# Optimization experiments

Hardware: AMD Instinct MI355X
Metric: run time of the kernel (lower is better)

The kernel has to match this reference:

```python
import jax, jax.numpy as jnp
import numpy as np

B, N, C = 8, 16384, 512

def setup_inputs() -> dict:
    key = jax.random.key(0)
    k1, k2 = jax.random.split(key)
    x = jax.random.normal(k1, (B, N, C), dtype=jnp.float32)
    gamma = jax.random.normal(k2, (1,), dtype=jnp.float32)
    return {"x": x, "gamma": gamma}

def reference(x, gamma):
    # x: [B, N, C]; torch code permutes to [B, C, N] for q/k/v
    v = jnp.transpose(x, (0, 2, 1))            # [B, C, N]
    # energy[b, i, j] = sum_n v[b, i, n] * v[b, j, n]  -> [B, C, C]
    energy = jnp.einsum('bin,bjn->bij', v, v)
    # max-subtract-then-negate score transform
    energy_new = jnp.max(energy, axis=-1, keepdims=True) - energy
    attention = jax.nn.softmax(energy_new, axis=-1)   # [B, C, C]
    out = jnp.einsum('bij,bjn->bin', attention, v)    # [B, C, N]
    out = gamma * out + v
    return jnp.transpose(out, (0, 2, 1))              # [B, N, C]
```

## Files before the change

### kernel.cpp

```cpp
#include <hip/hip_runtime.h>
#include <hip/hip_fp16.h>
#include <stdint.h>

#define B_ 8
#define N_ 16384
#define C_ 512
#define KS 16

typedef _Float16 h16;
typedef _Float16 half8 __attribute__((ext_vector_type(8)));
typedef float f32x4 __attribute__((ext_vector_type(4)));

__device__ __forceinline__ void gload16(const void* g, void* l) {
  __builtin_amdgcn_global_load_lds(
      (const __attribute__((address_space(1))) uint32_t*)g,
      (__attribute__((address_space(3))) uint32_t*)l, 16, 0, 0);
}

__device__ __forceinline__ half8 ldfrag(const h16* t, int r, int g) {
  return *(const half8*)(t + r * 32 + ((g ^ ((r >> 1) & 3)) << 3));
}

__global__ __launch_bounds__(256) void k_prep(const float* __restrict__ x,
    h16* __restrict__ xtH, h16* __restrict__ xtL, h16* __restrict__ xh, int b0) {
  int bl = blockIdx.z, b = b0 + bl;
  int n0 = blockIdx.x << 6, c0 = blockIdx.y << 6;
  __shared__ __align__(16) h16 lh[64][70];
  __shared__ __align__(16) h16 ll[64][70];
  int t = threadIdx.x;
  const float* xp = x + ((size_t)b * N_ + n0) * C_ + c0;
  h16* xhp = xh + ((size_t)bl * N_ + n0) * C_ + c0;
#pragma unroll
  for (int it = 0; it < 4; ++it) {
    int nr = (t >> 4) + (it << 4);
    int c4 = (t & 15) << 2;
    f32x4 v = *(const f32x4*)(xp + (size_t)nr * C_ + c4);
    h16 hv[4], lv[4];
#pragma unroll
    for (int u = 0; u < 4; ++u) {
      h16 h = (h16)v[u];
      hv[u] = h;
      lv[u] = (h16)(v[u] - (float)h);
    }
    union { h16 a[4]; uint2 u2; } ph;
    ph.a[0] = hv[0]; ph.a[1] = hv[1]; ph.a[2] = hv[2]; ph.a[3] = hv[3];
    *(uint2*)(xhp + (size_t)nr * C_ + c4) = ph.u2;
#pragma unroll
    for (int u = 0; u < 4; ++u) { lh[c4 + u][nr] = hv[u]; ll[c4 + u][nr] = lv[u]; }
  }
  __syncthreads();
  int cr = t >> 2, ns = (t & 3) << 4;
  size_t ob = ((size_t)bl * C_ + c0 + cr) * N_ + n0 + ns;
  uint32_t rh[8], rl[8];
#pragma unroll
  for (int e = 0; e < 8; ++e) {
    rh[e] = *(const uint32_t*)&lh[cr][ns + 2 * e];
    rl[e] = *(const uint32_t*)&ll[cr][ns + 2 * e];
  }
  *(uint4*)(xtH + ob)     = make_uint4(rh[0], rh[1], rh[2], rh[3]);
  *(uint4*)(xtH + ob + 8) = make_uint4(rh[4], rh[5], rh[6], rh[7]);
  *(uint4*)(xtL + ob)     = make_uint4(rl[0], rl[1], rl[2], rl[3]);
  *(uint4*)(xtL + ob + 8) = make_uint4(rl[4], rl[5], rl[6], rl[7]);
}

__global__ __launch_bounds__(256) void k_gram(const h16* __restrict__ xtH,
    const h16* __restrict__ xtL, float* __restrict__ Ep, int nb) {
  int NW = gridDim.x;
  int b = blockIdx.x;
  int L = (b & 7) * (NW >> 3) + (b >> 3);
  int tp = L % 10;
  int pair = L / 10;
  int kq = pair & (KS - 1);
  int bl = pair / KS;
  int ti = 0, rem = tp;
  while (rem >= 4 - ti) { rem -= 4 - ti; ++ti; }
  int tj = ti + rem;
  int i0 = ti << 7, j0 = tj << 7;
  bool diag = (ti == tj);
  int k0 = kq * (N_ / KS);
  __shared__ __align__(16) h16 lds[4 * 4096];
  const h16* bHi = xtH + ((size_t)bl * C_ + i0) * N_;
  const h16* bLi = xtL + ((size_t)bl * C_ + i0) * N_;
  const h16* bHj = xtH + ((size_t)bl * C_ + j0) * N_;
  const h16* bLj = xtL + ((size_t)bl * C_ + j0) * N_;
  int tid = threadIdx.x, lane = tid & 63, wid = tid >> 6;
  int wr = (wid >> 1) << 6, wc = (wid & 1) << 6;
  int r16 = lane & 15, g = lane >> 4;
  f32x4 acc[4][4] = {};
  const h16* pHi = lds;
  const h16* pLi = lds + 4096;
  const h16* pHj = diag ? lds : lds + 8192;
  const h16* pLj = diag ? lds + 4096 : lds + 12288;
  int r0 = tid >> 2, s = tid & 3;
  int r1 = r0 + 64;
  int sx0 = (s ^ ((r0 >> 1) & 3)) << 3, sx1 = (s ^ ((r1 >> 1) & 3)) << 3;
  int d0 = r0 * 32 + s * 8, d1 = r1 * 32 + s * 8;
  for (int kc = 0; kc < N_ / KS / 32; ++kc) {
    int k = k0 + (kc << 5);
    __syncthreads();
    gload16(bHi + (size_t)r0 * N_ + k + sx0, (void*)(lds + d0));
    gload16(bHi + (size_t)r1 * N_ + k + sx1, (void*)(lds + d1));
    gload16(bLi + (size_t)r0 * N_ + k + sx0, (void*)(lds + 4096 + d0));
    gload16(bLi + (size_t)r1 * N_ + k + sx1, (void*)(lds + 4096 + d1));
    if (!diag) {
      gload16(bHj + (size_t)r0 * N_ + k + sx0, (void*)(lds + 8192 + d0));
      gload16(bHj + (size_t)r1 * N_ + k + sx1, (void*)(lds + 8192 + d1));
      gload16(bLj + (size_t)r0 * N_ + k + sx0, (void*)(lds + 12288 + d0));
      gload16(bLj + (size_t)r1 * N_ + k + sx1, (void*)(lds + 12288 + d1));
    }
    __syncthreads();
    half8 ahi[4], ali[4], bhj[4], blj[4];
#pragma unroll
    for (int m = 0; m < 4; ++m) {
      int ra = wr + (m << 4) + r16;
      int rb = wc + (m << 4) + r16;
      ahi[m] = ldfrag(pHi, ra, g);
      ali[m] = ldfrag(pLi, ra, g);
      bhj[m] = ldfrag(pHj, rb, g);
      blj[m] = ldfrag(pLj, rb, g);
    }
#pragma unroll
    for (int m = 0; m < 4; ++m)
#pragma unroll
      for (int n = 0; n < 4; ++n) {
        acc[m][n] = __builtin_amdgcn_mfma_f32_16x16x32_f16(ahi[m], bhj[n], acc[m][n], 0, 0, 0);
        acc[m][n] = __builtin_amdgcn_mfma_f32_16x16x32_f16(ahi[m], blj[n], acc[m][n], 0, 0, 0);
        acc[m][n] = __builtin_amdgcn_mfma_f32_16x16x32_f16(ali[m], bhj[n], acc[m][n], 0, 0, 0);
      }
  }
  float* e = Ep + (size_t)(kq * nb + bl) * C_ * C_;
#pragma unroll
  for (int m = 0; m < 4; ++m)
#pragma unroll
    for (int n = 0; n < 4; ++n)
#pragma unroll
      for (int q = 0; q < 4; ++q) {
        int i = i0 + wr + (m << 4) + (g << 2) + q;
        int j = j0 + wc + (n << 4) + r16;
        float v = acc[m][n][q];
        e[(size_t)i * C_ + j] = v;
        if (!diag) e[(size_t)j * C_ + i] = v;
      }
}

__global__ __launch_bounds__(256) void k_smax(const float* __restrict__ Ep,
    const float* __restrict__ gamma, h16* __restrict__ Wt, int nb) {
  int row = (blockIdx.x << 2) + (threadIdx.x >> 6);
  int lane = threadIdx.x & 63;
  int bl = row >> 9, i = row & 511;
  size_t st = (size_t)nb * C_ * C_;
  const float* e = Ep + ((size_t)bl * C_ + i) * C_;
  f32x4 a = *(const f32x4*)(e + (lane << 2));
  f32x4 b = *(const f32x4*)(e + 256 + (lane << 2));
#pragma unroll
  for (int kq = 1; kq < KS; ++kq) {
    a += *(const f32x4*)(e + kq * st + (lane << 2));
    b += *(const f32x4*)(e + kq * st + 256 + (lane << 2));
  }
  float mx = fmaxf(fmaxf(fmaxf(a[0], a[1]), fmaxf(a[2], a[3])),
                   fmaxf(fmaxf(b[0], b[1]), fmaxf(b[2], b[3])));
#pragma unroll
  for (int d = 32; d; d >>= 1) mx = fmaxf(mx, __shfl_xor(mx, d));
  f32x4 ta, tb;
#pragma unroll
  for (int u = 0; u < 4; ++u) { ta[u] = mx - a[u]; tb[u] = mx - b[u]; }
  float tm = fmaxf(fmaxf(fmaxf(ta[0], ta[1]), fmaxf(ta[2], ta[3])),
                   fmaxf(fmaxf(tb[0], tb[1]), fmaxf(tb[2], tb[3])));
#pragma unroll
  for (int d = 32; d; d >>= 1) tm = fmaxf(tm, __shfl_xor(tm, d));
  f32x4 pa, pb;
#pragma unroll
  for (int u = 0; u < 4; ++u) { pa[u] = expf(ta[u] - tm); pb[u] = expf(tb[u] - tm); }
  float sm = pa[0] + pa[1] + pa[2] + pa[3] + pb[0] + pb[1] + pb[2] + pb[3];
#pragma unroll
  for (int d = 32; d; d >>= 1) sm += __shfl_xor(sm, d);
  float w = gamma[0] / sm;
  union { h16 a4[4]; uint2 u2; } o0, o1;
#pragma unroll
  for (int u = 0; u < 4; ++u) { o0.a4[u] = (h16)(pa[u] * w); o1.a4[u] = (h16)(pb[u] * w); }
  h16* wp = Wt + ((size_t)bl * C_ + i) * C_;
  *(uint2*)(wp + (lane << 2)) = o0.u2;
  *(uint2*)(wp + 256 + (lane << 2)) = o1.u2;
}

__global__ __launch_bounds__(512) void k_out(const h16* __restrict__ xh,
    const h16* __restrict__ Wt, const float* __restrict__ x,
    float* __restrict__ y, int b0) {
  int NW = gridDim.x;
  int bswz = blockIdx.x;
  int L = (bswz & 7) * (NW >> 3) + (bswz >> 3);
  int bl = L >> 8;
  int rem2 = L & 255;
  int ct = rem2 & 1, nt = rem2 >> 1;
  int b = b0 + bl;
  int n0 = nt << 7, c0 = ct << 8;
  __shared__ __align__(16) h16 shA[4096];
  __shared__ __align__(16) h16 shB[8192];
  int tid = threadIdx.x, lane = tid & 63, wid = tid >> 6;
  int wn = (wid >> 2) << 6, wc = (wid & 3) << 6;
  int r16 = lane & 15, g = lane >> 4;
  const h16* bA = xh + ((size_t)bl * N_ + n0) * C_;
  const h16* bB = Wt + ((size_t)bl * C_ + c0) * C_;
  f32x4 acc[4][4] = {};
  int rA = tid >> 2, s4 = tid & 3;
  int rB1 = rA + 128;
  int sxA = (s4 ^ ((rA >> 1) & 3)) << 3;
  int sxB1 = (s4 ^ ((rB1 >> 1) & 3)) << 3;
  for (int kc = 0; kc < C_ / 32; ++kc) {
    int k = kc << 5;
    __syncthreads();
    gload16(bA + (size_t)rA * C_ + k + sxA, (void*)(shA + rA * 32 + s4 * 8));
    gload16(bB + (size_t)rA * C_ + k + sxA, (void*)(shB + rA * 32 + s4 * 8));
    gload16(bB + (size_t)rB1 * C_ + k + sxB1, (void*)(shB + rB1 * 32 + s4 * 8));
    __syncthreads();
    half8 af[4], bf[4];
#pragma unroll
    for (int m = 0; m < 4; ++m) {
      af[m] = ldfrag(shA, wn + (m << 4) + r16, g);
      bf[m] = ldfrag(shB, wc + (m << 4) + r16, g);
    }
#pragma unroll
    for (int m = 0; m < 4; ++m)
#pragma unroll
      for (int n = 0; n < 4; ++n)
        acc[m][n] = __builtin_amdgcn_mfma_f32_16x16x32_f16(af[m], bf[n], acc[m][n], 0, 0, 0);
  }
  const float* xp = x + ((size_t)b * N_ + n0) * C_;
  float* yp = y + ((size_t)b * N_ + n0) * C_;
#pragma unroll
  for (int m = 0; m < 4; ++m)
#pragma unroll
    for (int n = 0; n < 4; ++n)
#pragma unroll
      for (int q = 0; q < 4; ++q) {
        int nn = wn + (m << 4) + (g << 2) + q;
        size_t idx = (size_t)nn * C_ + c0 + wc + (n << 4) + r16;
        yp[idx] = acc[m][n][q] + xp[idx];
      }
}

extern "C" void kernel_launch(void* const* d_in, const int* in_sizes, int n_in,
                              void* d_out, int out_size, void* d_ws, size_t ws_size,
                              hipStream_t stream) {
  const float* x = (const float*)d_in[0];
  const float* gamma = (const float*)d_in[1];
  float* y = (float*)d_out;
  const size_t szXT = (size_t)C_ * N_ * sizeof(h16);
  const size_t szXH = (size_t)N_ * C_ * sizeof(h16);
  const size_t szEP = (size_t)KS * C_ * C_ * sizeof(float);
  const size_t szWT = (size_t)C_ * C_ * sizeof(h16);
  const size_t per = 2 * szXT + szXH + szEP + szWT;
  int nb = B_;
  while (nb > 1 && (size_t)nb * per > ws_size) nb >>= 1;
  if (nb < 1) nb = 1;
  char* p = (char*)d_ws;
  h16* xtH = (h16*)p; p += (size_t)nb * szXT;
  h16* xtL = (h16*)p; p += (size_t)nb * szXT;
  h16* xh  = (h16*)p; p += (size_t)nb * szXH;
  float* Ep = (float*)p; p += (size_t)nb * szEP;
  h16* Wt  = (h16*)p;
  for (int b0 = 0; b0 < B_; b0 += nb) {
    k_prep<<<dim3(N_ / 64, C_ / 64, nb), 256, 0, stream>>>(x, xtH, xtL, xh, b0);
    k_gram<<<dim3(nb * KS * 10), 256, 0, stream>>>(xtH, xtL, Ep, nb);
    k_smax<<<dim3(nb * (C_ / 4)), 256, 0, stream>>>(Ep, gamma, Wt, nb);
    k_out<<<dim3(nb * 256), 512, 0, stream>>>(xh, Wt, x, y, b0);
  }
}
```

Measured before the change: 799.6 us.

## Double-buffer LDS tiles in gram and output GEMM kernels

Adds a second LDS buffer to both the gram kernel and the output GEMM kernel. The next K-chunk is issued with global_load_lds while the MFMAs run on the current buffer, which removes one barrier per iteration and hides load latency. LDS use doubles (64KB in gram), which can lower occupancy. The global_load_lds writes may also need explicit vmcnt waits before the barrier to be correct.

```diff
diff --git a/kernel.cpp b/kernel.cpp
--- a/kernel.cpp
+++ b/kernel.cpp
@@ -78,7 +78,8 @@
   int i0 = ti << 7, j0 = tj << 7;
   bool diag = (ti == tj);
   int k0 = kq * (N_ / KS);
-  __shared__ __align__(16) h16 lds[4 * 4096];
+  __shared__ __align__(16) h16 ldsA[4 * 4096];
+  __shared__ __align__(16) h16 ldsB[4 * 4096];
   const h16* bHi = xtH + ((size_t)bl * C_ + i0) * N_;
   const h16* bLi = xtL + ((size_t)bl * C_ + i0) * N_;
   const h16* bHj = xtH + ((size_t)bl * C_ + j0) * N_;
@@ -87,28 +88,28 @@
   int wr = (wid >> 1) << 6, wc = (wid & 1) << 6;
   int r16 = lane & 15, g = lane >> 4;
   f32x4 acc[4][4] = {};
-  const h16* pHi = lds;
-  const h16* pLi = lds + 4096;
-  const h16* pHj = diag ? lds : lds + 8192;
-  const h16* pLj = diag ? lds + 4096 : lds + 12288;
   int r0 = tid >> 2, s = tid & 3;
   int r1 = r0 + 64;
   int sx0 = (s ^ ((r0 >> 1) & 3)) << 3, sx1 = (s ^ ((r1 >> 1) & 3)) << 3;
   int d0 = r0 * 32 + s * 8, d1 = r1 * 32 + s * 8;
-  for (int kc = 0; kc < N_ / KS / 32; ++kc) {
-    int k = k0 + (kc << 5);
-    __syncthreads();
-    gload16(bHi + (size_t)r0 * N_ + k + sx0, (void*)(lds + d0));
-    gload16(bHi + (size_t)r1 * N_ + k + sx1, (void*)(lds + d1));
-    gload16(bLi + (size_t)r0 * N_ + k + sx0, (void*)(lds + 4096 + d0));
-    gload16(bLi + (size_t)r1 * N_ + k + sx1, (void*)(lds + 4096 + d1));
+
+  auto stage = [&](h16* base, int k) {
+    gload16(bHi + (size_t)r0 * N_ + k + sx0, (void*)(base + d0));
+    gload16(bHi + (size_t)r1 * N_ + k + sx1, (void*)(base + d1));
+    gload16(bLi + (size_t)r0 * N_ + k + sx0, (void*)(base + 4096 + d0));
+    gload16(bLi + (size_t)r1 * N_ + k + sx1, (void*)(base + 4096 + d1));
     if (!diag) {
-      gload16(bHj + (size_t)r0 * N_ + k + sx0, (void*)(lds + 8192 + d0));
-      gload16(bHj + (size_t)r1 * N_ + k + sx1, (void*)(lds + 8192 + d1));
-      gload16(bLj + (size_t)r0 * N_ + k + sx0, (void*)(lds + 12288 + d0));
-      gload16(bLj + (size_t)r1 * N_ + k + sx1, (void*)(lds + 12288 + d1));
-    }
-    __syncthreads();
+      gload16(bHj + (size_t)r0 * N_ + k + sx0, (void*)(base + 8192 + d0));
+      gload16(bHj + (size_t)r1 * N_ + k + sx1, (void*)(base + 8192 + d1));
+      gload16(bLj + (size_t)r0 * N_ + k + sx0, (void*)(base + 12288 + d0));
+      gload16(bLj + (size_t)r1 * N_ + k + sx1, (void*)(base + 12288 + d1));
+    }
+  };
+  auto compute = [&](const h16* base) {
+    const h16* pHi = base;
+    const h16* pLi = base + 4096;
+    const h16* pHj = diag ? base : base + 8192;
+    const h16* pLj = diag ? base + 4096 : base + 12288;
     half8 ahi[4], ali[4], bhj[4], blj[4];
 #pragma unroll
     for (int m = 0; m < 4; ++m) {
@@ -127,7 +128,20 @@
         acc[m][n] = __builtin_amdgcn_mfma_f32_16x16x32_f16(ahi[m], blj[n], acc[m][n], 0, 0, 0);
         acc[m][n] = __builtin_amdgcn_mfma_f32_16x16x32_f16(ali[m], bhj[n], acc[m][n], 0, 0, 0);
       }
-  }
+  };
+
+  const int NT = N_ / KS / 32;
+  stage(ldsA, k0);
+  __syncthreads();
+  for (int kc = 0; kc < NT; kc += 2) {
+    stage(ldsB, k0 + ((kc + 1) << 5));
+    compute(ldsA);
+    __syncthreads();
+    if (kc + 2 < NT) stage(ldsA, k0 + ((kc + 2) << 5));
+    compute(ldsB);
+    __syncthreads();
+  }
+
   float* e = Ep + (size_t)(kq * nb + bl) * C_ * C_;
 #pragma unroll
   for (int m = 0; m < 4; ++m)
@@ -194,8 +208,10 @@
   int ct = rem2 & 1, nt = rem2 >> 1;
   int b = b0 + bl;
   int n0 = nt << 7, c0 = ct << 8;
-  __shared__ __align__(16) h16 shA[4096];
-  __shared__ __align__(16) h16 shB[8192];
+  __shared__ __align__(16) h16 shA_A[4096];
+  __shared__ __align__(16) h16 shB_A[8192];
+  __shared__ __align__(16) h16 shA_B[4096];
+  __shared__ __align__(16) h16 shB_B[8192];
   int tid = threadIdx.x, lane = tid & 63, wid = tid >> 6;
   int wn = (wid >> 2) << 6, wc = (wid & 3) << 6;
   int r16 = lane & 15, g = lane >> 4;
@@ -206,25 +222,39 @@
   int rB1 = rA + 128;
   int sxA = (s4 ^ ((rA >> 1) & 3)) << 3;
   int sxB1 = (s4 ^ ((rB1 >> 1) & 3)) << 3;
-  for (int kc = 0; kc < C_ / 32; ++kc) {
-    int k = kc << 5;
-    __syncthreads();
-    gload16(bA + (size_t)rA * C_ + k + sxA, (void*)(shA + rA * 32 + s4 * 8));
-    gload16(bB + (size_t)rA * C_ + k + sxA, (void*)(shB + rA * 32 + s4 * 8));
-    gload16(bB + (size_t)rB1 * C_ + k + sxB1, (void*)(shB + rB1 * 32 + s4 * 8));
-    __syncthreads();
+  int dA = rA * 32 + s4 * 8, dB1 = rB1 * 32 + s4 * 8;
+
+  auto stage = [&](h16* sa, h16* sb, int k) {
+    gload16(bA + (size_t)rA * C_ + k + sxA, (void*)(sa + dA));
+    gload16(bB + (size_t)rA * C_ + k + sxA, (void*)(sb + dA));
+    gload16(bB + (size_t)rB1 * C_ + k + sxB1, (void*)(sb + dB1));
+  };
+  auto compute = [&](const h16* sa, const h16* sb) {
     half8 af[4], bf[4];
 #pragma unroll
     for (int m = 0; m < 4; ++m) {
-      af[m] = ldfrag(shA, wn + (m << 4) + r16, g);
-      bf[m] = ldfrag(shB, wc + (m << 4) + r16, g);
+      af[m] = ldfrag(sa, wn + (m << 4) + r16, g);
+      bf[m] = ldfrag(sb, wc + (m << 4) + r16, g);
     }
 #pragma unroll
     for (int m = 0; m < 4; ++m)
 #pragma unroll
       for (int n = 0; n < 4; ++n)
         acc[m][n] = __builtin_amdgcn_mfma_f32_16x16x32_f16(af[m], bf[n], acc[m][n], 0, 0, 0);
-  }
+  };
+
+  const int NT = C_ / 32;
+  stage(shA_A, shB_A, 0);
+  __syncthreads();
+  for (int kc = 0; kc < NT; kc += 2) {
+    stage(shA_B, shB_B, (kc + 1) << 5);
+    compute(shA_A, shB_A);
+    __syncthreads();
+    if (kc + 2 < NT) stage(shA_A, shB_A, (kc + 2) << 5);
+    compute(shA_B, shB_B);
+    __syncthreads();
+  }
+
   const float* xp = x + ((size_t)b * N_ + n0) * C_;
   float* yp = y + ((size_t)b * N_ + n0) * C_;
 #pragma unroll
```

Measured after the change: 899.6 us. 1.12x slower.
